# Kernel optimization log

Hardware: AMD Instinct MI355X
Metric: run time of the kernel (lower is better)

Reference implementation:

```python
import jax, jax.numpy as jnp
import numpy as np

HEAD_DIM = 6
WS = 8  # window size
GROUPS = 4
EPS = 1e-5


def conv3x3(x, w, b):
    y = jax.lax.conv_general_dilated(x, w, (1, 1), [(1, 1), (1, 1)],
                                     dimension_numbers=('NCHW', 'OIHW', 'NCHW'))
    return y + b[None, :, None, None]


def conv1x1(x, w, b):
    # w: (O, C, 1, 1) pointwise conv == channel matmul
    return jnp.einsum('bchw,oc->bohw', x, w[:, :, 0, 0]) + b[None, :, None, None]


def group_norm(x, gamma, beta):
    B, C, H, W = x.shape
    xg = x.reshape(B, GROUPS, C // GROUPS, H, W)
    mu = xg.mean(axis=(2, 3, 4), keepdims=True)
    var = xg.var(axis=(2, 3, 4), keepdims=True)
    xg = (xg - mu) * jax.lax.rsqrt(var + EPS)
    return xg.reshape(B, C, H, W) * gamma[None, :, None, None] + beta[None, :, None, None]


def window_attention(x, qkv_w, qkv_b, proj_w, proj_b):
    # Per-window channel attention (attn is head_dim x head_dim, softmax over last dim).
    B, C, H, W = x.shape
    heads = C // HEAD_DIM
    scale = HEAD_DIM ** -0.5
    Hn, Wn = H // WS, W // WS
    L = WS * WS
    qkv = conv1x1(x, qkv_w, qkv_b)                       # (B, 3C, H, W); 1x1 conv commutes with windowing
    qkv = qkv.reshape(B, 3, heads, HEAD_DIM, Hn, WS, Wn, WS)
    qkv = qkv.transpose(1, 0, 4, 6, 2, 3, 5, 7).reshape(3, B, Hn, Wn, heads, HEAD_DIM, L)
    q, k, v = qkv[0], qkv[1], qkv[2]
    attn = jnp.einsum('bijhdl,bijhel->bijhde', q, k) * scale  # (B,Hn,Wn,heads,hd,hd)
    attn = jax.nn.softmax(attn, axis=-1)
    out = jnp.einsum('bijhde,bijhel->bijhdl', attn, v)
    out = out.reshape(B, Hn, Wn, heads, HEAD_DIM, WS, WS)
    out = out.transpose(0, 3, 4, 1, 5, 2, 6).reshape(B, C, H, W)
    return conv1x1(out, proj_w, proj_b)


def shifted_window_attention(x, qkv_w, qkv_b, proj_w, proj_b):
    B, C, H, W = x.shape
    pad_h = (WS - H % WS) % WS
    pad_w = (WS - W % WS) % WS
    if pad_h or pad_w:
        x = jnp.pad(x, ((0, 0), (0, 0), (0, pad_h), (0, pad_w)), mode='reflect')
    s = WS // 2
    x_sh = jnp.roll(x, shift=(-s, -s), axis=(2, 3))
    x1 = window_attention(x, qkv_w, qkv_b, proj_w, proj_b)
    x2 = window_attention(x_sh, qkv_w, qkv_b, proj_w, proj_b)
    x2 = jnp.roll(x2, shift=(s, s), axis=(2, 3))
    x = (x1 + x2) * 0.5
    return x[:, :, :H, :W]


def setup_inputs() -> dict:
    key = jax.random.key(0)
    ks = jax.random.split(key, 12)
    B, Cin, Cout, T, H, W = 16, 96, 96, 256, 128, 128
    std = 0.05
    return {
        'x': jax.random.normal(ks[0], (B, Cin, H, W), jnp.float32),
        't_emb': jax.random.normal(ks[1], (B, T), jnp.float32),
        'w1': jax.random.normal(ks[2], (Cout, Cin, 3, 3), jnp.float32) * std,
        'b1': jnp.zeros((Cout,), jnp.float32),
        'g1': jnp.ones((Cout,), jnp.float32),
        'be1': jnp.zeros((Cout,), jnp.float32),
        'wt': jax.random.normal(ks[3], (2 * Cout, T), jnp.float32) * std,
        'bt': jnp.zeros((2 * Cout,), jnp.float32),
        'qkv_w': jax.random.normal(ks[4], (3 * Cout, Cout, 1, 1), jnp.float32) * std,
        'qkv_b': jnp.zeros((3 * Cout,), jnp.float32),
        'proj_w': jax.random.normal(ks[5], (Cout, Cout, 1, 1), jnp.float32) * std,
        'proj_b': jnp.zeros((Cout,), jnp.float32),
        'ga': jnp.ones((Cout,), jnp.float32),
        'ba': jnp.zeros((Cout,), jnp.float32),
        'w2': jax.random.normal(ks[6], (Cout, Cout, 3, 3), jnp.float32) * std,
        'b2': jnp.zeros((Cout,), jnp.float32),
        'g2': jnp.ones((Cout,), jnp.float32),
        'be2': jnp.zeros((Cout,), jnp.float32),
    }


def reference(x, t_emb, w1, b1, g1, be1, wt, bt, qkv_w, qkv_b, proj_w, proj_b,
              ga, ba, w2, b2, g2, be2):
    C = w1.shape[0]
    # layer1: conv3x3 -> GN(4) -> SiLU
    h = jax.nn.silu(group_norm(conv3x3(x, w1, b1), g1, be1))
    # time FiLM
    t = jax.nn.silu(t_emb @ wt.T + bt)             # (B, 2C)
    shift, bias = t[:, :C], t[:, C:]
    h = h * (1.0 + shift[:, :, None, None]) + bias[:, :, None, None]
    residual = h
    h = group_norm(h, ga, ba)
    h = shifted_window_attention(h, qkv_w, qkv_b, proj_w, proj_b)
    h = residual + h
    # layer2: conv3x3 -> GN(4) -> SiLU
    h = jax.nn.silu(group_norm(conv3x3(h, w2, b2), g2, be2))
    return h
```

## Files before the change

### kernel.cpp

```cpp
#include <hip/hip_runtime.h>

#define B_   16
#define C_   96
#define H_   128
#define W_   128
#define HW_  16384
#define CPG_ 24
#define NPG_ 393216.0f
#define TDIM_ 256
#define PLANE_ ((size_t)B_ * C_ * HW_)

typedef unsigned short ushort_t;
typedef __bf16 bf16x8 __attribute__((ext_vector_type(8)));
typedef float  f32x4  __attribute__((ext_vector_type(4)));
typedef unsigned short u16x8 __attribute__((ext_vector_type(8)));
typedef unsigned short u16x4 __attribute__((ext_vector_type(4)));

#define ICP 104

__device__ __forceinline__ float silu_f(float x) { return x / (1.f + __expf(-x)); }
__device__ __forceinline__ float bf2f(ushort_t u) {
    union { float f; unsigned int i; } x; x.i = ((unsigned int)u) << 16; return x.f;
}
__device__ __forceinline__ ushort_t f2bf(float f) {
    __bf16 h = (__bf16)f; return *(ushort_t*)&h;
}

__global__ void temb_kernel(const float* __restrict__ t_emb,
                            const float* __restrict__ wt,
                            const float* __restrict__ bt,
                            float* __restrict__ tvec) {
    int idx = blockIdx.x * 256 + threadIdx.x;
    if (idx >= B_ * 192) return;
    int b = idx / 192, o = idx - b * 192;
    float a = bt[o];
    const float* te = t_emb + b * TDIM_;
    const float* wr = wt + o * TDIM_;
    for (int k = 0; k < TDIM_; ++k) a += te[k] * wr[k];
    tvec[idx] = silu_f(a);
}

__global__ void castw_kernel(const float* __restrict__ w1,
                             const float* __restrict__ w2,
                             ushort_t* __restrict__ wbf1,
                             ushort_t* __restrict__ wbf2) {
    int i = blockIdx.x * 256 + threadIdx.x;
    int j    = i & 7;
    int lane = (i >> 3) & 63;
    int t    = i >> 9;
    int nt   = t % 6;
    int ks   = t / 6;
    int kk   = ks / 3, ck = ks - 3 * kk;
    int oc = nt * 16 + (lane & 15);
    int ic = ck * 32 + (lane >> 4) * 8 + j;
    int src = (oc * 96 + ic) * 9 + kk;
    wbf1[i] = f2bf(w1[src]);
    wbf2[i] = f2bf(w2[src]);
}

template<int FP32>
__device__ __forceinline__ void stage_row(const void* __restrict__ xin,
                                          ushort_t* __restrict__ ti2,
                                          int b, int gy, int x0, int slot, int tid) {
    const bool rowok = (gy >= 0 && gy < H_);
#pragma unroll
    for (int it = 0; it < 3; ++it) {
        int idx = it * 256 + tid;
        int ic = idx % 96;
        int xc = idx / 96;
        u16x8 v = {};
        if (rowok) {
            if (FP32) {
                const float* xf = (const float*)xin;
                const float4* p = (const float4*)&xf[((size_t)(b * 96 + ic) * H_ + gy) * W_ + x0 + xc * 8];
                float4 f0 = p[0], f1 = p[1];
                v[0] = f2bf(f0.x); v[1] = f2bf(f0.y); v[2] = f2bf(f0.z); v[3] = f2bf(f0.w);
                v[4] = f2bf(f1.x); v[5] = f2bf(f1.y); v[6] = f2bf(f1.z); v[7] = f2bf(f1.w);
            } else {
                const ushort_t* xb = (const ushort_t*)xin;
                v = *(const u16x8*)&xb[((size_t)(b * 96 + ic) * H_ + gy) * W_ + x0 + xc * 8];
            }
        }
        ushort_t* dst = &ti2[(slot * 66 + xc * 8 + 1) * ICP + ic];
#pragma unroll
        for (int j = 0; j < 8; ++j) dst[j * ICP] = v[j];
    }
    if (tid < 192) {
        int ic = tid % 96;
        int side = tid / 96;
        int xi = side ? 65 : 0;
        int gx = x0 - 1 + xi;
        ushort_t vv = 0;
        if (rowok && gx >= 0 && gx < W_) {
            if (FP32) vv = f2bf(((const float*)xin)[((size_t)(b * 96 + ic) * H_ + gy) * W_ + gx]);
            else      vv = ((const ushort_t*)xin)[((size_t)(b * 96 + ic) * H_ + gy) * W_ + gx];
        }
        ti2[(slot * 66 + xi) * ICP + ic] = vv;
    }
}

template<int FP32>
__global__ __launch_bounds__(256, 2)
void conv3x3_mfma_kernel(const void* __restrict__ xin,
                         const ushort_t* __restrict__ wbf,
                         const float* __restrict__ bias,
                         float* __restrict__ out,
                         float* __restrict__ stats) {
    __shared__ __align__(16) ushort_t ti2[4 * 66 * ICP];
    __shared__ float red[4][96][2];

    const int b   = blockIdx.z;
    const int y0  = blockIdx.y * 4;
    const int x0  = blockIdx.x * 64;
    const int tid = threadIdx.x;
    const int wv   = tid >> 6;
    const int lane = tid & 63;
    const int l15  = lane & 15;
    const int quad = lane >> 4;

    stage_row<FP32>(xin, ti2, b, y0 - 1, x0, 0, tid);
    stage_row<FP32>(xin, ti2, b, y0 + 0, x0, 1, tid);
    stage_row<FP32>(xin, ti2, b, y0 + 1, x0, 2, tid);
    stage_row<FP32>(xin, ti2, b, y0 + 2, x0, 3, tid);

    const ushort_t* wrp = wbf + (size_t)lane * 8;

    bf16x8 wA[6], wB[6];
#pragma unroll
    for (int nt = 0; nt < 6; ++nt)
        wA[nt] = *(const bf16x8*)&wrp[nt * 512];

    f32x4 acc[4][6];
#pragma unroll
    for (int m = 0; m < 4; ++m)
#pragma unroll
        for (int nt = 0; nt < 6; ++nt)
            acc[m][nt] = (f32x4){0.f, 0.f, 0.f, 0.f};

    __syncthreads();

    auto body = [&](int ks, bf16x8 (&cur)[6], bf16x8 (&nxt)[6]) {
        const int kk = ks / 3, ck = ks - 3 * kk;
        const int ky = kk / 3, kx = kk - 3 * ky;
        if (ks < 26) {
#pragma unroll
            for (int nt = 0; nt < 6; ++nt)
                nxt[nt] = *(const bf16x8*)&wrp[((ks + 1) * 6 + nt) * 512];
        }
        const int kbase = ck * 32 + quad * 8;
        bf16x8 a[4];
#pragma unroll
        for (int m = 0; m < 4; ++m) {
            const int slot = (m + ky) & 3;
            a[m] = *(const bf16x8*)&ti2[(slot * 66 + wv * 16 + l15 + kx) * ICP + kbase];
        }
#pragma unroll
        for (int nt = 0; nt < 6; ++nt)
#pragma unroll
            for (int m = 0; m < 4; ++m)
                acc[m][nt] = __builtin_amdgcn_mfma_f32_16x16x32_bf16(a[m], cur[nt], acc[m][nt], 0, 0, 0);
    };

#pragma unroll
    for (int ks = 0; ks < 27; ++ks) {
        if (ks == 9) {
            __syncthreads();
            stage_row<FP32>(xin, ti2, b, y0 + 3, x0, 0, tid);
            __syncthreads();
        }
        if (ks == 18) {
            __syncthreads();
            stage_row<FP32>(xin, ti2, b, y0 + 4, x0, 1, tid);
            __syncthreads();
        }
        if (ks & 1) body(ks, wB, wA);
        else        body(ks, wA, wB);
    }

    float lsum[6], lsq[6];
#pragma unroll
    for (int nt = 0; nt < 6; ++nt) { lsum[nt] = 0.f; lsq[nt] = 0.f; }

#pragma unroll
    for (int m = 0; m < 4; ++m) {
        const int gy = y0 + m;
        const int gx = x0 + wv * 16 + quad * 4;
#pragma unroll
        for (int nt = 0; nt < 6; ++nt) {
            const int oc = nt * 16 + l15;
            const float bz = bias[oc];
            float v0 = acc[m][nt][0] + bz;
            float v1 = acc[m][nt][1] + bz;
            float v2 = acc[m][nt][2] + bz;
            float v3 = acc[m][nt][3] + bz;
            float4 vv = make_float4(v0, v1, v2, v3);
            *(float4*)&out[((size_t)(b * 96 + oc) * H_ + gy) * W_ + gx] = vv;
            lsum[nt] += v0 + v1 + v2 + v3;
            lsq[nt]  += v0 * v0 + v1 * v1 + v2 * v2 + v3 * v3;
        }
    }
#pragma unroll
    for (int nt = 0; nt < 6; ++nt) {
        float s = lsum[nt], q = lsq[nt];
        s += __shfl_down(s, 32, 64);
        s += __shfl_down(s, 16, 64);
        q += __shfl_down(q, 32, 64);
        q += __shfl_down(q, 16, 64);
        if (lane < 16) {
            red[wv][nt * 16 + lane][0] = s;
            red[wv][nt * 16 + lane][1] = q;
        }
    }
    __syncthreads();
    if (tid < 8) {
        const int g = tid >> 1, which = tid & 1;
        float v = 0.f;
        for (int oc = g * CPG_; oc < g * CPG_ + CPG_; ++oc)
            for (int w2 = 0; w2 < 4; ++w2) v += red[w2][oc][which];
        atomicAdd(&stats[(b * 4 + g) * 2 + which], v);
    }
}

__global__ void apply1_kernel(const float* y,
                              const float* __restrict__ stats1,
                              const float* __restrict__ g1,
                              const float* __restrict__ be1,
                              const float* __restrict__ tvec,
                              float* h,
                              float* __restrict__ stats2) {
    const int bc = blockIdx.x;
    const int b = bc / C_, c = bc - b * C_;
    const int g = c / CPG_;
    const float sum = stats1[(b * 4 + g) * 2], sumsq = stats1[(b * 4 + g) * 2 + 1];
    const float mean = sum / NPG_;
    const float var  = sumsq / NPG_ - mean * mean;
    const float rstd = rsqrtf(var + 1e-5f);
    const float sc = rstd * g1[c];
    const float sh = be1[c] - mean * sc;
    const float tsc = 1.f + tvec[b * 192 + c];
    const float tbi = tvec[b * 192 + 96 + c];

    const float4* yp = (const float4*)(y + (size_t)bc * HW_);
    float4* hp = (float4*)(h + (size_t)bc * HW_);
    float ls = 0.f, lss = 0.f;
    for (int i = threadIdx.x; i < HW_ / 4; i += 256) {
        float4 v = yp[i];
        float r0 = silu_f(v.x * sc + sh) * tsc + tbi;
        float r1 = silu_f(v.y * sc + sh) * tsc + tbi;
        float r2 = silu_f(v.z * sc + sh) * tsc + tbi;
        float r3 = silu_f(v.w * sc + sh) * tsc + tbi;
        hp[i] = make_float4(r0, r1, r2, r3);
        ls  += r0 + r1 + r2 + r3;
        lss += r0*r0 + r1*r1 + r2*r2 + r3*r3;
    }
    for (int off = 32; off > 0; off >>= 1) {
        ls  += __shfl_down(ls, off, 64);
        lss += __shfl_down(lss, off, 64);
    }
    if ((threadIdx.x & 63) == 0) {
        atomicAdd(&stats2[(b * 4 + g) * 2 + 0], ls);
        atomicAdd(&stats2[(b * 4 + g) * 2 + 1], lss);
    }
}

__global__ void gn_bf16_kernel(const float* __restrict__ in,
                               const float* __restrict__ stats,
                               const float* __restrict__ gamma,
                               const float* __restrict__ beta,
                               ushort_t* __restrict__ outb) {
    const int bc = blockIdx.x;
    const int b = bc / C_, c = bc - b * C_;
    const int g = c / CPG_;
    const float sum = stats[(b * 4 + g) * 2], sumsq = stats[(b * 4 + g) * 2 + 1];
    const float mean = sum / NPG_;
    const float var  = sumsq / NPG_ - mean * mean;
    const float rstd = rsqrtf(var + 1e-5f);
    const float sc = rstd * gamma[c];
    const float sh = beta[c] - mean * sc;
    const float4* ip = (const float4*)(in + (size_t)bc * HW_);
    ushort4* op = (ushort4*)(outb + (size_t)bc * HW_);
    for (int i = threadIdx.x; i < HW_ / 4; i += 256) {
        float4 v = ip[i];
        ushort4 u = { f2bf(v.x * sc + sh), f2bf(v.y * sc + sh),
                      f2bf(v.z * sc + sh), f2bf(v.w * sc + sh) };
        op[i] = u;
    }
}

__global__ void gn_apply_kernel(const float* in,
                                const float* __restrict__ stats,
                                const float* __restrict__ gamma,
                                const float* __restrict__ beta,
                                float* out, int dosilu) {
    const int bc = blockIdx.x;
    const int b = bc / C_, c = bc - b * C_;
    const int g = c / CPG_;
    const float sum = stats[(b * 4 + g) * 2], sumsq = stats[(b * 4 + g) * 2 + 1];
    const float mean = sum / NPG_;
    const float var  = sumsq / NPG_ - mean * mean;
    const float rstd = rsqrtf(var + 1e-5f);
    const float sc = rstd * gamma[c];
    const float sh = beta[c] - mean * sc;
    const float4* ip = (const float4*)(in + (size_t)bc * HW_);
    float4* op = (float4*)(out + (size_t)bc * HW_);
    for (int i = threadIdx.x; i < HW_ / 4; i += 256) {
        float4 v = ip[i];
        float r0 = v.x * sc + sh, r1 = v.y * sc + sh;
        float r2 = v.z * sc + sh, r3 = v.w * sc + sh;
        if (dosilu) { r0 = silu_f(r0); r1 = silu_f(r1); r2 = silu_f(r2); r3 = silu_f(r3); }
        op[i] = make_float4(r0, r1, r2, r3);
    }
}

__global__ __launch_bounds__(256, 3)
void qkv_gemm_kernel(const ushort_t* __restrict__ xq,
                     const float* __restrict__ qw,
                     const float* __restrict__ qb,
                     ushort_t* __restrict__ qkvbuf) {
    __shared__ __align__(16) ushort_t ti[2 * 64 * ICP];
    __shared__ __align__(16) ushort_t wc[96 * ICP];

    const int bz = blockIdx.z;
    const int b = bz / 3, s = bz - b * 3;
    const int y0 = blockIdx.y * 2;
    const int x0 = blockIdx.x * 64;
    const int tid = threadIdx.x;
    const int wv = tid >> 6, lane = tid & 63;
    const int l15 = lane & 15, quad = lane >> 4;

#pragma unroll
    for (int it = 0; it < 6; ++it) {
        int idx = it * 256 + tid;
        int ic = idx % 96;
        int t2 = idx / 96;
        int xc = t2 & 7;
        int r  = t2 >> 3;
        u16x8 v = *(const u16x8*)&xq[((size_t)(b * 96 + ic) * H_ + y0 + r) * W_ + x0 + xc * 8];
        ushort_t* dst = &ti[(r * 64 + xc * 8) * ICP + ic];
#pragma unroll
        for (int j = 0; j < 8; ++j) dst[j * ICP] = v[j];
    }
#pragma unroll
    for (int it = 0; it < 9; ++it) {
        int idx = it * 256 + tid;
        int icq = idx % 24;
        int oc  = idx / 24;
        float4 wv4 = *(const float4*)&qw[(s * 96 + oc) * 96 + icq * 4];
        ushort4 u = { f2bf(wv4.x), f2bf(wv4.y), f2bf(wv4.z), f2bf(wv4.w) };
        *(ushort4*)&wc[oc * ICP + icq * 4] = u;
    }
    __syncthreads();

    f32x4 acc[2][6];
#pragma unroll
    for (int m = 0; m < 2; ++m)
#pragma unroll
        for (int nt = 0; nt < 6; ++nt) acc[m][nt] = (f32x4){0.f, 0.f, 0.f, 0.f};

#pragma unroll
    for (int ck = 0; ck < 3; ++ck) {
        const int kbase = ck * 32 + quad * 8;
        bf16x8 a0 = *(const bf16x8*)&ti[(0 * 64 + wv * 16 + l15) * ICP + kbase];
        bf16x8 a1 = *(const bf16x8*)&ti[(1 * 64 + wv * 16 + l15) * ICP + kbase];
#pragma unroll
        for (int nt = 0; nt < 6; ++nt) {
            bf16x8 bv = *(const bf16x8*)&wc[(nt * 16 + l15) * ICP + kbase];
            acc[0][nt] = __builtin_amdgcn_mfma_f32_16x16x32_bf16(a0, bv, acc[0][nt], 0, 0, 0);
            acc[1][nt] = __builtin_amdgcn_mfma_f32_16x16x32_bf16(a1, bv, acc[1][nt], 0, 0, 0);
        }
    }

#pragma unroll
    for (int m = 0; m < 2; ++m) {
        const int gy = y0 + m;
        const int gx = x0 + wv * 16 + quad * 4;
#pragma unroll
        for (int nt = 0; nt < 6; ++nt) {
            const int ocg = s * 96 + nt * 16 + l15;
            const float bz2 = qb[ocg];
            ushort4 u = { f2bf(acc[m][nt][0] + bz2), f2bf(acc[m][nt][1] + bz2),
                          f2bf(acc[m][nt][2] + bz2), f2bf(acc[m][nt][3] + bz2) };
            *(ushort4*)&qkvbuf[((size_t)(b * 288 + ocg) * H_ + gy) * W_ + gx] = u;
        }
    }
}

#define QKC 1288
#define QKR 160
#define OSTS 1032
#define VTS 520
__global__ __launch_bounds__(256, 2)
void attn2_kernel(const ushort_t* __restrict__ qkv,
                  ushort_t* __restrict__ obuf, int shift, int accumulate) {
    __shared__ __align__(16) ushort_t qk[12 * QKC];
    __shared__ __align__(16) ushort_t vt[16 * VTS + 32];
    __shared__ __align__(16) ushort_t ost[6 * OSTS];

    const int h = blockIdx.x, wy = blockIdx.y, b = blockIdx.z;
    const int tid = threadIdx.x;
    const int wv = tid >> 6, lane = tid & 63;
    const int l15 = lane & 15, quad = lane >> 4;

    for (int idx = tid; idx < 2304; idx += 256) {
        int xc = idx & 15;
        int t2 = idx >> 4;
        int r  = t2 & 7;
        int ch = t2 >> 3;
        int part = ch / 6, d = ch - part * 6;
        int gch = part * 96 + h * 6 + d;
        int gy = (wy * 8 + r + shift) & 127;
        size_t rowb = ((size_t)(b * 288 + gch) * H_ + gy) * W_;
        ushort4 u0, u1;
        if (shift == 0) {
            u0 = *(const ushort4*)&qkv[rowb + xc * 8];
            u1 = *(const ushort4*)&qkv[rowb + xc * 8 + 4];
        } else {
            u0 = *(const ushort4*)&qkv[rowb + ((xc * 8 + 4) & 127)];
            u1 = *(const ushort4*)&qkv[rowb + ((xc * 8 + 8) & 127)];
        }
        ushort_t* dst = (part < 2) ? &qk[ch * QKC + r * QKR + xc * 8]
                                   : &ost[d * OSTS + r * 128 + xc * 8];
        *(ushort4*)dst = u0;
        *(ushort4*)(dst + 4) = u1;
    }
    __syncthreads();

    {
        const int r   = tid >> 5;
        const int pxq = tid & 31;
        const int px  = pxq * 4;
        u16x4 vv[6];
#pragma unroll
        for (int c = 0; c < 6; ++c)
            vv[c] = *(const u16x4*)&ost[c * OSTS + r * 128 + px];
        const int wx = px >> 3;
        const int p7 = px & 7;
#pragma unroll
        for (int j = 0; j < 4; ++j) {
            u16x8 t;
            t[0] = vv[0][j]; t[1] = vv[1][j]; t[2] = vv[2][j];
            t[3] = vv[3][j]; t[4] = vv[4][j]; t[5] = vv[5][j];
            t[6] = 0; t[7] = 0;
            *(u16x8*)&vt[wx * VTS + (r * 8 + p7 + j) * 8] = t;
        }
        if (tid < 16) ((unsigned int*)(vt + 16 * VTS))[tid] = 0u;
    }
    __syncthreads();

    const float scale = 0.40824829046386302f;
    const int dcl = (l15 < 6) ? l15 : 5;
    const int chA = 6 + dcl;
    const int chB = dcl;

    for (int i = 0; i < 4; ++i) {
        const int wx = wv * 4 + i;
        f32x4 sa = (f32x4){0.f, 0.f, 0.f, 0.f};
#pragma unroll
        for (int ck = 0; ck < 2; ++ck) {
            const int r = ck * 4 + quad;
            bf16x8 af  = *(const bf16x8*)&qk[chA * QKC + r * QKR + wx * 8];
            bf16x8 bfv = *(const bf16x8*)&qk[chB * QKC + r * QKR + wx * 8];
            sa = __builtin_amdgcn_mfma_f32_16x16x32_bf16(af, bfv, sa, 0, 0, 0);
        }
        float s0 = sa[0] * scale, s1 = sa[1] * scale, s2 = sa[2] * scale, s3 = sa[3] * scale;
        float m = -3.4e38f;
        if (quad == 0) m = fmaxf(fmaxf(s0, s1), fmaxf(s2, s3));
        else if (quad == 1) m = fmaxf(s0, s1);
        m = fmaxf(m, __shfl_xor(m, 16, 64));
        m = fmaxf(m, __shfl_xor(m, 32, 64));
        float p0 = (quad <= 1) ? __expf(s0 - m) : 0.f;
        float p1 = (quad <= 1) ? __expf(s1 - m) : 0.f;
        float p2 = (quad == 0) ? __expf(s2 - m) : 0.f;
        float p3 = (quad == 0) ? __expf(s3 - m) : 0.f;
        float sum = p0 + p1 + p2 + p3;
        sum += __shfl_xor(sum, 16, 64);
        sum += __shfl_xor(sum, 32, 64);
        float inv = 1.f / sum;
        p0 *= inv; p1 *= inv; p2 *= inv; p3 *= inv;
        float e4 = __shfl_xor(p0, 16, 64);
        float e5 = __shfl_xor(p1, 16, 64);
        bf16x8 pf;
        pf[0] = (__bf16)p0; pf[1] = (__bf16)p1; pf[2] = (__bf16)p2; pf[3] = (__bf16)p3;
        pf[4] = (__bf16)e4; pf[5] = (__bf16)e5;
        pf[6] = (__bf16)0.f; pf[7] = (__bf16)0.f;
        if (quad != 0) { bf16x8 z = {}; pf = z; }
#pragma unroll
        for (int mt = 0; mt < 4; ++mt) {
            bf16x8 av = *(const bf16x8*)&vt[wx * VTS + (mt * 16 + l15) * 8 + quad * 8];
            f32x4 o = __builtin_amdgcn_mfma_f32_16x16x32_bf16(av, pf, (f32x4){0.f,0.f,0.f,0.f}, 0, 0, 0);
            if (l15 < 6) {
                const int px = mt * 16 + quad * 4;
                const int r = px >> 3, c = px & 7;
                ushort4 st = { f2bf(o[0]), f2bf(o[1]), f2bf(o[2]), f2bf(o[3]) };
                *(ushort4*)&ost[l15 * OSTS + r * 128 + wx * 8 + c] = st;
            }
        }
    }
    __syncthreads();

    for (int idx = tid; idx < 768; idx += 256) {
        int xc = idx & 15;
        int t2 = idx >> 4;
        int r = t2 & 7, d = t2 >> 3;
        int gy = (wy * 8 + r + shift) & 127;
        size_t rowb = ((size_t)(b * 96 + h * 6 + d) * H_ + gy) * W_;
        size_t a0, a1;
        if (shift == 0) { a0 = rowb + xc * 8; a1 = rowb + xc * 8 + 4; }
        else { a0 = rowb + ((xc * 8 + 4) & 127); a1 = rowb + ((xc * 8 + 8) & 127); }
        const ushort_t* src = &ost[d * OSTS + r * 128 + xc * 8];
        ushort4 v0 = *(const ushort4*)src;
        ushort4 v1 = *(const ushort4*)(src + 4);
        if (accumulate) {
            ushort4 q0 = *(const ushort4*)&obuf[a0];
            ushort4 q1 = *(const ushort4*)&obuf[a1];
            v0.x = f2bf(0.5f * (bf2f(v0.x) + bf2f(q0.x)));
            v0.y = f2bf(0.5f * (bf2f(v0.y) + bf2f(q0.y)));
            v0.z = f2bf(0.5f * (bf2f(v0.z) + bf2f(q0.z)));
            v0.w = f2bf(0.5f * (bf2f(v0.w) + bf2f(q0.w)));
            v1.x = f2bf(0.5f * (bf2f(v1.x) + bf2f(q1.x)));
            v1.y = f2bf(0.5f * (bf2f(v1.y) + bf2f(q1.y)));
            v1.z = f2bf(0.5f * (bf2f(v1.z) + bf2f(q1.z)));
            v1.w = f2bf(0.5f * (bf2f(v1.w) + bf2f(q1.w)));
        }
        *(ushort4*)&obuf[a0] = v0;
        *(ushort4*)&obuf[a1] = v1;
    }
}

__global__ __launch_bounds__(256, 3)
void proj_gemm_kernel(const ushort_t* __restrict__ ob,
                      const float* __restrict__ pw,
                      const float* __restrict__ pb,
                      const float* __restrict__ resid,
                      ushort_t* __restrict__ h2) {
    __shared__ __align__(16) ushort_t ti[2 * 64 * ICP];
    __shared__ __align__(16) ushort_t wc[96 * ICP];

    const int b = blockIdx.z;
    const int y0 = blockIdx.y * 2;
    const int x0 = blockIdx.x * 64;
    const int tid = threadIdx.x;
    const int wv = tid >> 6, lane = tid & 63;
    const int l15 = lane & 15, quad = lane >> 4;

#pragma unroll
    for (int it = 0; it < 6; ++it) {
        int idx = it * 256 + tid;
        int ic = idx % 96;
        int t2 = idx / 96;
        int xc = t2 & 7;
        int r  = t2 >> 3;
        u16x8 v = *(const u16x8*)&ob[((size_t)(b * 96 + ic) * H_ + y0 + r) * W_ + x0 + xc * 8];
        ushort_t* dst = &ti[(r * 64 + xc * 8) * ICP + ic];
#pragma unroll
        for (int j = 0; j < 8; ++j) dst[j * ICP] = v[j];
    }
#pragma unroll
    for (int it = 0; it < 9; ++it) {
        int idx = it * 256 + tid;
        int icq = idx % 24;
        int oc  = idx / 24;
        float4 wv4 = *(const float4*)&pw[oc * 96 + icq * 4];
        ushort4 u = { f2bf(wv4.x), f2bf(wv4.y), f2bf(wv4.z), f2bf(wv4.w) };
        *(ushort4*)&wc[oc * ICP + icq * 4] = u;
    }
    __syncthreads();

    f32x4 acc[2][6];
#pragma unroll
    for (int m = 0; m < 2; ++m)
#pragma unroll
        for (int nt = 0; nt < 6; ++nt) acc[m][nt] = (f32x4){0.f, 0.f, 0.f, 0.f};

#pragma unroll
    for (int ck = 0; ck < 3; ++ck) {
        const int kbase = ck * 32 + quad * 8;
        bf16x8 a0 = *(const bf16x8*)&ti[(0 * 64 + wv * 16 + l15) * ICP + kbase];
        bf16x8 a1 = *(const bf16x8*)&ti[(1 * 64 + wv * 16 + l15) * ICP + kbase];
#pragma unroll
        for (int nt = 0; nt < 6; ++nt) {
            bf16x8 bv = *(const bf16x8*)&wc[(nt * 16 + l15) * ICP + kbase];
            acc[0][nt] = __builtin_amdgcn_mfma_f32_16x16x32_bf16(a0, bv, acc[0][nt], 0, 0, 0);
            acc[1][nt] = __builtin_amdgcn_mfma_f32_16x16x32_bf16(a1, bv, acc[1][nt], 0, 0, 0);
        }
    }

#pragma unroll
    for (int m = 0; m < 2; ++m) {
        const int gy = y0 + m;
        const int gx = x0 + wv * 16 + quad * 4;
#pragma unroll
        for (int nt = 0; nt < 6; ++nt) {
            const int oc = nt * 16 + l15;
            const float bz2 = pb[oc];
            size_t addr = ((size_t)(b * 96 + oc) * H_ + gy) * W_ + gx;
            float4 rv = *(const float4*)&resid[addr];
            ushort4 u = { f2bf(acc[m][nt][0] + bz2 + rv.x),
                          f2bf(acc[m][nt][1] + bz2 + rv.y),
                          f2bf(acc[m][nt][2] + bz2 + rv.z),
                          f2bf(acc[m][nt][3] + bz2 + rv.w) };
            *(ushort4*)&h2[addr] = u;
        }
    }
}

extern "C" void kernel_launch(void* const* d_in, const int* in_sizes, int n_in,
                              void* d_out, int out_size, void* d_ws, size_t ws_size,
                              hipStream_t stream) {
    const float* x     = (const float*)d_in[0];
    const float* t_emb = (const float*)d_in[1];
    const float* w1    = (const float*)d_in[2];
    const float* b1    = (const float*)d_in[3];
    const float* g1    = (const float*)d_in[4];
    const float* be1   = (const float*)d_in[5];
    const float* wt    = (const float*)d_in[6];
    const float* bt    = (const float*)d_in[7];
    const float* qkv_w = (const float*)d_in[8];
    const float* qkv_b = (const float*)d_in[9];
    const float* proj_w= (const float*)d_in[10];
    const float* proj_b= (const float*)d_in[11];
    const float* ga    = (const float*)d_in[12];
    const float* ba    = (const float*)d_in[13];
    const float* w2    = (const float*)d_in[14];
    const float* b2    = (const float*)d_in[15];
    const float* g2    = (const float*)d_in[16];
    const float* be2   = (const float*)d_in[17];

    float* out = (float*)d_out;

    ushort_t* A  = (ushort_t*)d_ws;
    ushort_t* Bq = A + PLANE_;
    float* stats = (float*)(Bq + 3 * PLANE_);
    float* tvec  = stats + 384;
    ushort_t* wbf1 = (ushort_t*)(tvec + 3072);
    ushort_t* wbf2 = wbf1 + 82944;

    hipMemsetAsync(stats, 0, 384 * sizeof(float), stream);
    temb_kernel<<<12, 256, 0, stream>>>(t_emb, wt, bt, tvec);
    castw_kernel<<<324, 256, 0, stream>>>(w1, w2, wbf1, wbf2);

    conv3x3_mfma_kernel<1><<<dim3(2, 32, 16), 256, 0, stream>>>((const void*)x, wbf1, b1, out, stats);

    apply1_kernel<<<B_ * C_, 256, 0, stream>>>(out, stats, g1, be1, tvec, out, stats + 128);
    gn_bf16_kernel<<<B_ * C_, 256, 0, stream>>>(out, stats + 128, ga, ba, A);

    qkv_gemm_kernel<<<dim3(2, 64, 48), 256, 0, stream>>>(A, qkv_w, qkv_b, Bq);

    attn2_kernel<<<dim3(16, 16, 16), 256, 0, stream>>>(Bq, A, 0, 0);
    attn2_kernel<<<dim3(16, 16, 16), 256, 0, stream>>>(Bq, A, 4, 1);

    proj_gemm_kernel<<<dim3(2, 64, 16), 256, 0, stream>>>(A, proj_w, proj_b, out, Bq);

    conv3x3_mfma_kernel<0><<<dim3(2, 32, 16), 256, 0, stream>>>((const void*)Bq, wbf2, b2, out, stats + 256);

    gn_apply_kernel<<<B_ * C_, 256, 0, stream>>>(out, stats + 256, g2, be2, out, 1);
}
```

Baseline: 738.3 us.

## Shrink conv3x3 row tile, prefetch halo rows via registers, reuse qkv input tile

The conv3x3 kernel now computes 2 output rows per block instead of 4, using a 3-slot LDS ring and launch bounds of 3 blocks per CU, with the grid doubled in y. The extra input row is loaded into registers early and written to LDS later, so its global load latency overlaps MFMA work instead of sitting between barriers. The qkv GEMM loops over the three q/k/v weight slices inside one block, so the staged input tile is reused instead of reloaded by three separate blocks. In exchange, the smaller conv tile reloads more halo rows per output row, and the qkv kernel now does its three slices serially within each block.

```diff
diff --git a/kernel.cpp b/kernel.cpp
--- a/kernel.cpp
+++ b/kernel.cpp
@@ -59,58 +59,74 @@
 }
 
 template<int FP32>
-__device__ __forceinline__ void stage_row(const void* __restrict__ xin,
-                                          ushort_t* __restrict__ ti2,
-                                          int b, int gy, int x0, int slot, int tid) {
+__device__ __forceinline__ void load_row(const void* __restrict__ xin,
+                                         int b, int gy, int x0, int tid,
+                                         u16x8 (&v)[3], ushort_t& halo) {
     const bool rowok = (gy >= 0 && gy < H_);
 #pragma unroll
     for (int it = 0; it < 3; ++it) {
         int idx = it * 256 + tid;
         int ic = idx % 96;
         int xc = idx / 96;
-        u16x8 v = {};
+        u16x8 t = {};
         if (rowok) {
             if (FP32) {
                 const float* xf = (const float*)xin;
                 const float4* p = (const float4*)&xf[((size_t)(b * 96 + ic) * H_ + gy) * W_ + x0 + xc * 8];
                 float4 f0 = p[0], f1 = p[1];
-                v[0] = f2bf(f0.x); v[1] = f2bf(f0.y); v[2] = f2bf(f0.z); v[3] = f2bf(f0.w);
-                v[4] = f2bf(f1.x); v[5] = f2bf(f1.y); v[6] = f2bf(f1.z); v[7] = f2bf(f1.w);
+                t[0] = f2bf(f0.x); t[1] = f2bf(f0.y); t[2] = f2bf(f0.z); t[3] = f2bf(f0.w);
+                t[4] = f2bf(f1.x); t[5] = f2bf(f1.y); t[6] = f2bf(f1.z); t[7] = f2bf(f1.w);
             } else {
                 const ushort_t* xb = (const ushort_t*)xin;
-                v = *(const u16x8*)&xb[((size_t)(b * 96 + ic) * H_ + gy) * W_ + x0 + xc * 8];
+                t = *(const u16x8*)&xb[((size_t)(b * 96 + ic) * H_ + gy) * W_ + x0 + xc * 8];
             }
         }
+        v[it] = t;
+    }
+    halo = 0;
+    if (tid < 192) {
+        int ic = tid % 96;
+        int side = tid / 96;
+        int gx = side ? (x0 + 64) : (x0 - 1);
+        if (rowok && gx >= 0 && gx < W_) {
+            if (FP32) halo = f2bf(((const float*)xin)[((size_t)(b * 96 + ic) * H_ + gy) * W_ + gx]);
+            else      halo = ((const ushort_t*)xin)[((size_t)(b * 96 + ic) * H_ + gy) * W_ + gx];
+        }
+    }
+}
+
+__device__ __forceinline__ void store_row(ushort_t* __restrict__ ti2,
+                                          int slot, int tid,
+                                          const u16x8 (&v)[3], ushort_t halo) {
+#pragma unroll
+    for (int it = 0; it < 3; ++it) {
+        int idx = it * 256 + tid;
+        int ic = idx % 96;
+        int xc = idx / 96;
         ushort_t* dst = &ti2[(slot * 66 + xc * 8 + 1) * ICP + ic];
 #pragma unroll
-        for (int j = 0; j < 8; ++j) dst[j * ICP] = v[j];
+        for (int j = 0; j < 8; ++j) dst[j * ICP] = v[it][j];
     }
     if (tid < 192) {
         int ic = tid % 96;
         int side = tid / 96;
         int xi = side ? 65 : 0;
-        int gx = x0 - 1 + xi;
-        ushort_t vv = 0;
-        if (rowok && gx >= 0 && gx < W_) {
-            if (FP32) vv = f2bf(((const float*)xin)[((size_t)(b * 96 + ic) * H_ + gy) * W_ + gx]);
-            else      vv = ((const ushort_t*)xin)[((size_t)(b * 96 + ic) * H_ + gy) * W_ + gx];
-        }
-        ti2[(slot * 66 + xi) * ICP + ic] = vv;
+        ti2[(slot * 66 + xi) * ICP + ic] = halo;
     }
 }
 
 template<int FP32>
-__global__ __launch_bounds__(256, 2)
+__global__ __launch_bounds__(256, 3)
 void conv3x3_mfma_kernel(const void* __restrict__ xin,
                          const ushort_t* __restrict__ wbf,
                          const float* __restrict__ bias,
                          float* __restrict__ out,
                          float* __restrict__ stats) {
-    __shared__ __align__(16) ushort_t ti2[4 * 66 * ICP];
+    __shared__ __align__(16) ushort_t ti2[3 * 66 * ICP];
     __shared__ float red[4][96][2];
 
     const int b   = blockIdx.z;
-    const int y0  = blockIdx.y * 4;
+    const int y0  = blockIdx.y * 2;
     const int x0  = blockIdx.x * 64;
     const int tid = threadIdx.x;
     const int wv   = tid >> 6;
@@ -118,10 +134,15 @@
     const int l15  = lane & 15;
     const int quad = lane >> 4;
 
-    stage_row<FP32>(xin, ti2, b, y0 - 1, x0, 0, tid);
-    stage_row<FP32>(xin, ti2, b, y0 + 0, x0, 1, tid);
-    stage_row<FP32>(xin, ti2, b, y0 + 1, x0, 2, tid);
-    stage_row<FP32>(xin, ti2, b, y0 + 2, x0, 3, tid);
+    {
+        u16x8 r0[3], r1[3], r2[3]; ushort_t h0, h1, h2;
+        load_row<FP32>(xin, b, y0 - 1, x0, tid, r0, h0);
+        load_row<FP32>(xin, b, y0 + 0, x0, tid, r1, h1);
+        load_row<FP32>(xin, b, y0 + 1, x0, tid, r2, h2);
+        store_row(ti2, 0, tid, r0, h0);
+        store_row(ti2, 1, tid, r1, h1);
+        store_row(ti2, 2, tid, r2, h2);
+    }
 
     const ushort_t* wrp = wbf + (size_t)lane * 8;
 
@@ -130,14 +151,16 @@
     for (int nt = 0; nt < 6; ++nt)
         wA[nt] = *(const bf16x8*)&wrp[nt * 512];
 
-    f32x4 acc[4][6];
-#pragma unroll
-    for (int m = 0; m < 4; ++m)
+    f32x4 acc[2][6];
+#pragma unroll
+    for (int m = 0; m < 2; ++m)
 #pragma unroll
         for (int nt = 0; nt < 6; ++nt)
             acc[m][nt] = (f32x4){0.f, 0.f, 0.f, 0.f};
 
     __syncthreads();
+
+    u16x8 r3[3]; ushort_t h3;
 
     auto body = [&](int ks, bf16x8 (&cur)[6], bf16x8 (&nxt)[6]) {
         const int kk = ks / 3, ck = ks - 3 * kk;
@@ -148,31 +171,22 @@
                 nxt[nt] = *(const bf16x8*)&wrp[((ks + 1) * 6 + nt) * 512];
         }
         const int kbase = ck * 32 + quad * 8;
-        bf16x8 a[4];
-#pragma unroll
-        for (int m = 0; m < 4; ++m) {
-            const int slot = (m + ky) & 3;
-            a[m] = *(const bf16x8*)&ti2[(slot * 66 + wv * 16 + l15 + kx) * ICP + kbase];
-        }
-#pragma unroll
-        for (int nt = 0; nt < 6; ++nt)
-#pragma unroll
-            for (int m = 0; m < 4; ++m)
-                acc[m][nt] = __builtin_amdgcn_mfma_f32_16x16x32_bf16(a[m], cur[nt], acc[m][nt], 0, 0, 0);
+        const int s0 = ky % 3, s1 = (ky + 1) % 3;
+        bf16x8 a0 = *(const bf16x8*)&ti2[(s0 * 66 + wv * 16 + l15 + kx) * ICP + kbase];
+        bf16x8 a1 = *(const bf16x8*)&ti2[(s1 * 66 + wv * 16 + l15 + kx) * ICP + kbase];
+#pragma unroll
+        for (int nt = 0; nt < 6; ++nt) {
+            acc[0][nt] = __builtin_amdgcn_mfma_f32_16x16x32_bf16(a0, cur[nt], acc[0][nt], 0, 0, 0);
+            acc[1][nt] = __builtin_amdgcn_mfma_f32_16x16x32_bf16(a1, cur[nt], acc[1][nt], 0, 0, 0);
+        }
     };
 
 #pragma unroll
     for (int ks = 0; ks < 27; ++ks) {
-        if (ks == 9) {
-            __syncthreads();
-            stage_row<FP32>(xin, ti2, b, y0 + 3, x0, 0, tid);
-            __syncthreads();
-        }
-        if (ks == 18) {
-            __syncthreads();
-            stage_row<FP32>(xin, ti2, b, y0 + 4, x0, 1, tid);
-            __syncthreads();
-        }
+        if (ks == 6)  load_row<FP32>(xin, b, y0 + 2, x0, tid, r3, h3);
+        if (ks == 12) __syncthreads();
+        if (ks == 17) store_row(ti2, 0, tid, r3, h3);
+        if (ks == 18) __syncthreads();
         if (ks & 1) body(ks, wB, wA);
         else        body(ks, wA, wB);
     }
@@ -182,7 +196,7 @@
     for (int nt = 0; nt < 6; ++nt) { lsum[nt] = 0.f; lsq[nt] = 0.f; }
 
 #pragma unroll
-    for (int m = 0; m < 4; ++m) {
+    for (int m = 0; m < 2; ++m) {
         const int gy = y0 + m;
         const int gx = x0 + wv * 16 + quad * 4;
 #pragma unroll
@@ -320,8 +334,7 @@
     __shared__ __align__(16) ushort_t ti[2 * 64 * ICP];
     __shared__ __align__(16) ushort_t wc[96 * ICP];
 
-    const int bz = blockIdx.z;
-    const int b = bz / 3, s = bz - b * 3;
+    const int b = blockIdx.z;
     const int y0 = blockIdx.y * 2;
     const int x0 = blockIdx.x * 64;
     const int tid = threadIdx.x;
@@ -340,47 +353,52 @@
 #pragma unroll
         for (int j = 0; j < 8; ++j) dst[j * ICP] = v[j];
     }
-#pragma unroll
-    for (int it = 0; it < 9; ++it) {
-        int idx = it * 256 + tid;
-        int icq = idx % 24;
-        int oc  = idx / 24;
-        float4 wv4 = *(const float4*)&qw[(s * 96 + oc) * 96 + icq * 4];
-        ushort4 u = { f2bf(wv4.x), f2bf(wv4.y), f2bf(wv4.z), f2bf(wv4.w) };
-        *(ushort4*)&wc[oc * ICP + icq * 4] = u;
-    }
-    __syncthreads();
-
-    f32x4 acc[2][6];
-#pragma unroll
-    for (int m = 0; m < 2; ++m)
-#pragma unroll
-        for (int nt = 0; nt < 6; ++nt) acc[m][nt] = (f32x4){0.f, 0.f, 0.f, 0.f};
-
-#pragma unroll
-    for (int ck = 0; ck < 3; ++ck) {
-        const int kbase = ck * 32 + quad * 8;
-        bf16x8 a0 = *(const bf16x8*)&ti[(0 * 64 + wv * 16 + l15) * ICP + kbase];
-        bf16x8 a1 = *(const bf16x8*)&ti[(1 * 64 + wv * 16 + l15) * ICP + kbase];
-#pragma unroll
-        for (int nt = 0; nt < 6; ++nt) {
-            bf16x8 bv = *(const bf16x8*)&wc[(nt * 16 + l15) * ICP + kbase];
-            acc[0][nt] = __builtin_amdgcn_mfma_f32_16x16x32_bf16(a0, bv, acc[0][nt], 0, 0, 0);
-            acc[1][nt] = __builtin_amdgcn_mfma_f32_16x16x32_bf16(a1, bv, acc[1][nt], 0, 0, 0);
-        }
-    }
-
-#pragma unroll
-    for (int m = 0; m < 2; ++m) {
-        const int gy = y0 + m;
-        const int gx = x0 + wv * 16 + quad * 4;
-#pragma unroll
-        for (int nt = 0; nt < 6; ++nt) {
-            const int ocg = s * 96 + nt * 16 + l15;
-            const float bz2 = qb[ocg];
-            ushort4 u = { f2bf(acc[m][nt][0] + bz2), f2bf(acc[m][nt][1] + bz2),
-                          f2bf(acc[m][nt][2] + bz2), f2bf(acc[m][nt][3] + bz2) };
-            *(ushort4*)&qkvbuf[((size_t)(b * 288 + ocg) * H_ + gy) * W_ + gx] = u;
+
+#pragma unroll 1
+    for (int s = 0; s < 3; ++s) {
+        if (s) __syncthreads();
+#pragma unroll
+        for (int it = 0; it < 9; ++it) {
+            int idx = it * 256 + tid;
+            int icq = idx % 24;
+            int oc  = idx / 24;
+            float4 wv4 = *(const float4*)&qw[(s * 96 + oc) * 96 + icq * 4];
+            ushort4 u = { f2bf(wv4.x), f2bf(wv4.y), f2bf(wv4.z), f2bf(wv4.w) };
+            *(ushort4*)&wc[oc * ICP + icq * 4] = u;
+        }
+        __syncthreads();
+
+        f32x4 acc[2][6];
+#pragma unroll
+        for (int m = 0; m < 2; ++m)
+#pragma unroll
+            for (int nt = 0; nt < 6; ++nt) acc[m][nt] = (f32x4){0.f, 0.f, 0.f, 0.f};
+
+#pragma unroll
+        for (int ck = 0; ck < 3; ++ck) {
+            const int kbase = ck * 32 + quad * 8;
+            bf16x8 a0 = *(const bf16x8*)&ti[(0 * 64 + wv * 16 + l15) * ICP + kbase];
+            bf16x8 a1 = *(const bf16x8*)&ti[(1 * 64 + wv * 16 + l15) * ICP + kbase];
+#pragma unroll
+            for (int nt = 0; nt < 6; ++nt) {
+                bf16x8 bv = *(const bf16x8*)&wc[(nt * 16 + l15) * ICP + kbase];
+                acc[0][nt] = __builtin_amdgcn_mfma_f32_16x16x32_bf16(a0, bv, acc[0][nt], 0, 0, 0);
+                acc[1][nt] = __builtin_amdgcn_mfma_f32_16x16x32_bf16(a1, bv, acc[1][nt], 0, 0, 0);
+            }
+        }
+
+#pragma unroll
+        for (int m = 0; m < 2; ++m) {
+            const int gy = y0 + m;
+            const int gx = x0 + wv * 16 + quad * 4;
+#pragma unroll
+            for (int nt = 0; nt < 6; ++nt) {
+                const int ocg = s * 96 + nt * 16 + l15;
+                const float bz2 = qb[ocg];
+                ushort4 u = { f2bf(acc[m][nt][0] + bz2), f2bf(acc[m][nt][1] + bz2),
+                              f2bf(acc[m][nt][2] + bz2), f2bf(acc[m][nt][3] + bz2) };
+                *(ushort4*)&qkvbuf[((size_t)(b * 288 + ocg) * H_ + gy) * W_ + gx] = u;
+            }
         }
     }
 }
@@ -639,19 +657,19 @@
     temb_kernel<<<12, 256, 0, stream>>>(t_emb, wt, bt, tvec);
     castw_kernel<<<324, 256, 0, stream>>>(w1, w2, wbf1, wbf2);
 
-    conv3x3_mfma_kernel<1><<<dim3(2, 32, 16), 256, 0, stream>>>((const void*)x, wbf1, b1, out, stats);
+    conv3x3_mfma_kernel<1><<<dim3(2, 64, 16), 256, 0, stream>>>((const void*)x, wbf1, b1, out, stats);
 
     apply1_kernel<<<B_ * C_, 256, 0, stream>>>(out, stats, g1, be1, tvec, out, stats + 128);
     gn_bf16_kernel<<<B_ * C_, 256, 0, stream>>>(out, stats + 128, ga, ba, A);
 
-    qkv_gemm_kernel<<<dim3(2, 64, 48), 256, 0, stream>>>(A, qkv_w, qkv_b, Bq);
+    qkv_gemm_kernel<<<dim3(2, 64, 16), 256, 0, stream>>>(A, qkv_w, qkv_b, Bq);
 
     attn2_kernel<<<dim3(16, 16, 16), 256, 0, stream>>>(Bq, A, 0, 0);
     attn2_kernel<<<dim3(16, 16, 16), 256, 0, stream>>>(Bq, A, 4, 1);
 
     proj_gemm_kernel<<<dim3(2, 64, 16), 256, 0, stream>>>(A, proj_w, proj_b, out, Bq);
 
-    conv3x3_mfma_kernel<0><<<dim3(2, 32, 16), 256, 0, stream>>>((const void*)Bq, wbf2, b2, out, stats + 256);
+    conv3x3_mfma_kernel<0><<<dim3(2, 64, 16), 256, 0, stream>>>((const void*)Bq, wbf2, b2, out, stats + 256);
 
     gn_apply_kernel<<<B_ * C_, 256, 0, stream>>>(out, stats + 256, g2, be2, out, 1);
 }
```

After: 747.1 us. No clear change (+1.2%).
